# Kernel tuning notes

Hardware: AMD Instinct MI355X
Metric: run time of the kernel (lower is better)

The kernel has to match this reference:

```python
import jax, jax.numpy as jnp
import numpy as np

N_NODES = 50000
N_EDGES = 800000
N_GRAPHS = 128
IN_DIM = 128
HID = 128
OUT = 64
N_CONV = 4
BN_EPS = 1e-5


def setup_inputs() -> dict:
    key = jax.random.key(0)
    ks = jax.random.split(key, 12)
    h = jax.random.normal(ks[0], (N_NODES, IN_DIM), jnp.float32)
    edge_src = jax.random.randint(ks[1], (N_EDGES,), 0, N_NODES)
    edge_dst = jax.random.randint(ks[2], (N_EDGES,), 0, N_NODES)
    graph_ids = jnp.sort(jax.random.randint(ks[3], (N_NODES,), 0, N_GRAPHS))
    s1 = 1.0 / np.sqrt(IN_DIM)
    W1 = jax.random.uniform(ks[4], (N_CONV, IN_DIM, HID), jnp.float32, -s1, s1)
    W2 = jax.random.uniform(ks[5], (N_CONV, HID, HID), jnp.float32, -s1, s1)
    bn1_g = jnp.ones((N_CONV, HID), jnp.float32)
    bn1_b = jnp.zeros((N_CONV, HID), jnp.float32)
    bn2_g = jnp.ones((N_CONV, HID), jnp.float32)
    bn2_b = jnp.zeros((N_CONV, HID), jnp.float32)
    predW = jax.random.uniform(ks[6], (5, HID, OUT), jnp.float32, -s1, s1)
    predb = jnp.zeros((5, OUT), jnp.float32)
    return dict(h=h, edge_src=edge_src, edge_dst=edge_dst, graph_ids=graph_ids,
                W1=W1, bn1_g=bn1_g, bn1_b=bn1_b, W2=W2, bn2_g=bn2_g, bn2_b=bn2_b,
                predW=predW, predb=predb)


def _batchnorm(x, g, b):
    # training-mode batchnorm over the node dimension (biased variance, as torch)
    m = jnp.mean(x, axis=0)
    v = jnp.mean(jnp.square(x - m), axis=0)
    return (x - m) * jax.lax.rsqrt(v + BN_EPS) * g + b


def reference(h, edge_src, edge_dst, graph_ids, W1, bn1_g, bn1_b, W2, bn2_g, bn2_b, predW, predb):
    hidden_rep = [h]
    for i in range(N_CONV):
        # GINConv, eps=0: aggregate neighbor sum, add self, apply MLP
        agg = jax.ops.segment_sum(h[edge_src], edge_dst, num_segments=N_NODES)
        z = agg + h  # [N, d]
        z = jnp.matmul(z, W1[i])
        z = jax.nn.relu(_batchnorm(z, bn1_g[i], bn1_b[i]))
        z = jnp.matmul(z, W2[i])
        # outer batchnorm + relu
        h = jax.nn.relu(_batchnorm(z, bn2_g[i], bn2_b[i]))
        hidden_rep.append(h)
    score = jnp.zeros((N_GRAPHS, OUT), jnp.float32)
    for i, hi in enumerate(hidden_rep):
        pooled = jax.ops.segment_sum(hi, graph_ids, num_segments=N_GRAPHS)  # [G, d]
        score = score + jnp.matmul(pooled, predW[i]) + predb[i]
    return score
```

## Files before the change

kernel.cpp:

```cpp
#include <hip/hip_runtime.h>

#define NN 50000
#define NE 800000
#define NG 128
#define DIM 128
#define OUTD 64
#define NCONV 4
#define NB 196
#define BN_EPS 1e-5f

typedef __attribute__((ext_vector_type(8))) short short8;
typedef __attribute__((ext_vector_type(4))) float f32x4;
union BF8 { uint4 u; short8 s; };

__device__ inline unsigned f2bf(float f) {
    unsigned u = __float_as_uint(f);
    return (u + 0x7FFFu + ((u >> 16) & 1u)) >> 16;
}
__device__ inline float bf_lo(unsigned u) { return __uint_as_float(u << 16); }
__device__ inline float bf_hi(unsigned u) { return __uint_as_float(u & 0xFFFF0000u); }

__global__ __launch_bounds__(256) void k_degree(const int* __restrict__ dst,
                                                int* __restrict__ deg)
{
    int e = blockIdx.x * 256 + threadIdx.x;
    if (e < NE) atomicAdd(&deg[dst[e]], 1);
}

__global__ __launch_bounds__(256) void k_scan1(const int* __restrict__ deg,
                                               int* __restrict__ bsum)
{
    __shared__ int part[256];
    int t = threadIdx.x, idx = blockIdx.x * 256 + t;
    int v = (idx < NN) ? deg[idx] : 0;
    part[t] = v;
    __syncthreads();
    #pragma unroll
    for (int off = 1; off < 256; off <<= 1) {
        int u = (t >= off) ? part[t - off] : 0;
        __syncthreads();
        part[t] += u;
        __syncthreads();
    }
    if (t == 255) bsum[blockIdx.x] = part[255];
}

__global__ __launch_bounds__(256) void k_scan2(const int* __restrict__ bsum,
                                               int* __restrict__ boff)
{
    __shared__ int part[256];
    int t = threadIdx.x;
    int v = (t < NB) ? bsum[t] : 0;
    part[t] = v;
    __syncthreads();
    #pragma unroll
    for (int off = 1; off < 256; off <<= 1) {
        int u = (t >= off) ? part[t - off] : 0;
        __syncthreads();
        part[t] += u;
        __syncthreads();
    }
    if (t < NB) boff[t] = part[t] - v;
}

__global__ __launch_bounds__(256) void k_scan3(const int* __restrict__ deg,
                                               const int* __restrict__ boff,
                                               int* __restrict__ rowptr,
                                               int* __restrict__ cursor)
{
    __shared__ int part[256];
    int t = threadIdx.x, idx = blockIdx.x * 256 + t;
    int v = (idx < NN) ? deg[idx] : 0;
    part[t] = v;
    __syncthreads();
    #pragma unroll
    for (int off = 1; off < 256; off <<= 1) {
        int u = (t >= off) ? part[t - off] : 0;
        __syncthreads();
        part[t] += u;
        __syncthreads();
    }
    if (idx < NN) {
        int excl = part[t] - v + boff[blockIdx.x];
        rowptr[idx] = excl;
        cursor[idx] = excl;
    }
    if (idx == 0) rowptr[NN] = NE;
}

__global__ __launch_bounds__(256) void k_fill(const int* __restrict__ src,
                                              const int* __restrict__ dst,
                                              int* __restrict__ cursor,
                                              int* __restrict__ csr)
{
    int e = blockIdx.x * 256 + threadIdx.x;
    if (e >= NE) return;
    int pos = atomicAdd(&cursor[dst[e]], 1);
    csr[pos] = src[e];
}

__global__ __launch_bounds__(256) void k_bounds(const int* __restrict__ gid,
                                                int* __restrict__ gstart)
{
    int n = blockIdx.x * 256 + threadIdx.x;
    if (n >= NN) return;
    int g = gid[n];
    int gp = (n == 0) ? -1 : gid[n - 1];
    for (int x = gp + 1; x <= g; ++x) gstart[x] = n;
    if (n == NN - 1)
        for (int x = g + 1; x <= NG; ++x) gstart[x] = NN;
}

__global__ __launch_bounds__(256) void k_wprep(const float* __restrict__ W1,
                                               const float* __restrict__ W2,
                                               unsigned short* __restrict__ Wbf)
{
    int tid = blockIdx.x * 256 + threadIdx.x;
    int l   = tid & 63;
    int ctg = (tid >> 6) & 7;
    int kk  = (tid >> 9) & 3;
    int mat = tid >> 11;
    const float* Ws = (mat < 4) ? (W1 + (size_t)mat * DIM * DIM)
                                : (W2 + (size_t)(mat - 4) * DIM * DIM);
    int col = ctg * 16 + (l & 15);
    int k0  = kk * 32 + (l >> 4) * 8;
    unsigned sh[8];
    #pragma unroll
    for (int j = 0; j < 8; ++j) sh[j] = f2bf(Ws[(size_t)(k0 + j) * DIM + col]);
    uint4 pk;
    pk.x = sh[0] | (sh[1] << 16); pk.y = sh[2] | (sh[3] << 16);
    pk.z = sh[4] | (sh[5] << 16); pk.w = sh[6] | (sh[7] << 16);
    ((uint4*)Wbf)[tid] = pk;
}

__global__ __launch_bounds__(256) void k_cvt(const float* __restrict__ in,
                                             unsigned short* __restrict__ outb)
{
    int idx = blockIdx.x * 256 + threadIdx.x;
    if (idx >= NN * DIM / 4) return;
    float4 v = ((const float4*)in)[idx];
    uint2 pk;
    pk.x = f2bf(v.x) | (f2bf(v.y) << 16);
    pk.y = f2bf(v.z) | (f2bf(v.w) << 16);
    ((uint2*)outb)[idx] = pk;
}

__device__ inline void bn_affine4(const float* __restrict__ sumP,
                                  const float* __restrict__ sqP,
                                  const float* __restrict__ gP,
                                  const float* __restrict__ bP,
                                  int ch0, float4& av, float4& cv)
{
    const float invM = 1.f / (float)NN;
    #pragma unroll
    for (int j = 0; j < 4; ++j) {
        int ch = ch0 + j;
        float m = sumP[ch] * invM;
        float var = sqP[ch] * invM - m * m;
        float s = gP[ch] * rsqrtf(var + BN_EPS);
        (&av.x)[j] = s;
        (&cv.x)[j] = bP[ch] - m * s;
    }
}

__device__ inline float4 aff_relu(float4 v, const float4 av, const float4 cv)
{
    v.x = fmaxf(fmaf(v.x, av.x, cv.x), 0.f);
    v.y = fmaxf(fmaf(v.y, av.y, cv.y), 0.f);
    v.z = fmaxf(fmaf(v.z, av.z, cv.z), 0.f);
    v.w = fmaxf(fmaf(v.w, av.w, cv.w), 0.f);
    return v;
}

__global__ __launch_bounds__(256) void k_gather_bf(
    const unsigned short* __restrict__ hbf,
    const int* __restrict__ rowptr, const int* __restrict__ csr,
    unsigned short* __restrict__ aggbf)
{
    int t = threadIdx.x;
    int n = blockIdx.x * 8 + (t >> 5);
    if (n >= NN) return;
    int l = t & 31;
    const uint2* hp = (const uint2*)hbf;
    uint2 v0 = hp[(size_t)n * 32 + l];
    float a0 = bf_lo(v0.x), a1 = bf_hi(v0.x), a2 = bf_lo(v0.y), a3 = bf_hi(v0.y);
    int p = rowptr[n], end = rowptr[n + 1];
    for (; p + 4 <= end; p += 4) {
        int s0 = csr[p], s1 = csr[p + 1], s2 = csr[p + 2], s3 = csr[p + 3];
        uint2 u0 = hp[(size_t)s0 * 32 + l];
        uint2 u1 = hp[(size_t)s1 * 32 + l];
        uint2 u2 = hp[(size_t)s2 * 32 + l];
        uint2 u3 = hp[(size_t)s3 * 32 + l];
        a0 += bf_lo(u0.x) + bf_lo(u1.x) + bf_lo(u2.x) + bf_lo(u3.x);
        a1 += bf_hi(u0.x) + bf_hi(u1.x) + bf_hi(u2.x) + bf_hi(u3.x);
        a2 += bf_lo(u0.y) + bf_lo(u1.y) + bf_lo(u2.y) + bf_lo(u3.y);
        a3 += bf_hi(u0.y) + bf_hi(u1.y) + bf_hi(u2.y) + bf_hi(u3.y);
    }
    for (; p < end; ++p) {
        uint2 u = hp[(size_t)csr[p] * 32 + l];
        a0 += bf_lo(u.x); a1 += bf_hi(u.x); a2 += bf_lo(u.y); a3 += bf_hi(u.y);
    }
    uint2 pk;
    pk.x = f2bf(a0) | (f2bf(a1) << 16);
    pk.y = f2bf(a2) | (f2bf(a3) << 16);
    ((uint2*)aggbf)[(size_t)n * 32 + l] = pk;
}

template<bool AFFINE, bool WRITEH>
__global__ __launch_bounds__(256) void k_poolseg(
    const float* __restrict__ z,
    const float* __restrict__ sumP, const float* __restrict__ sqP,
    const float* __restrict__ gP, const float* __restrict__ bP,
    const int* __restrict__ gstart, float* __restrict__ pooled,
    unsigned short* __restrict__ hbf)
{
    const int g = blockIdx.x >> 2, split = blockIdx.x & 3;
    const int s = gstart[g], e = gstart[g + 1];
    const int len = e - s;
    const int chunk = (len + 3) >> 2;
    const int rs = s + split * chunk;
    const int re = min(e, rs + chunk);
    const int c4 = threadIdx.x & 31, rl = threadIdx.x >> 5;
    float4 av, cv;
    if (AFFINE) bn_affine4(sumP, sqP, gP, bP, c4 * 4, av, cv);
    float4 acc = make_float4(0.f, 0.f, 0.f, 0.f);
    for (int r = rs + rl; r < re; r += 8) {
        float4 v = ((const float4*)z)[(size_t)r * 32 + c4];
        if (AFFINE) v = aff_relu(v, av, cv);
        if (WRITEH) {
            uint2 pk;
            pk.x = f2bf(v.x) | (f2bf(v.y) << 16);
            pk.y = f2bf(v.z) | (f2bf(v.w) << 16);
            ((uint2*)(hbf + (size_t)r * DIM))[c4] = pk;
        }
        acc.x += v.x; acc.y += v.y; acc.z += v.z; acc.w += v.w;
    }
    __shared__ float4 red[8][32];
    red[rl][c4] = acc;
    __syncthreads();
    if (rl == 0) {
        float4 s4 = red[0][c4];
        #pragma unroll
        for (int r8 = 1; r8 < 8; ++r8) {
            float4 u = red[r8][c4];
            s4.x += u.x; s4.y += u.y; s4.z += u.z; s4.w += u.w;
        }
        float* p = pooled + (size_t)g * DIM + c4 * 4;
        atomicAdd(p + 0, s4.x);
        atomicAdd(p + 1, s4.y);
        atomicAdd(p + 2, s4.z);
        atomicAdd(p + 3, s4.w);
    }
}

template<bool ABF16>
__global__ __launch_bounds__(256) void k_gemm_mfma(
    const void* __restrict__ Xv_,
    const float* __restrict__ sumP, const float* __restrict__ sqP,
    const float* __restrict__ gP, const float* __restrict__ bP,
    const unsigned short* __restrict__ Wbf,
    float* __restrict__ Z,
    float* __restrict__ colsum, float* __restrict__ colsq)
{
    __shared__ unsigned short a_lds[16 * 520];
    const int t = threadIdx.x;
    const int row0 = blockIdx.x * 64;
    const int q = t & 15;

    if (ABF16) {
        const unsigned short* Xb = (const unsigned short*)Xv_;
        #pragma unroll
        for (int it = 0; it < 4; ++it) {
            int id = t + it * 256;
            int row = id >> 4;
            int grow = row0 + row;
            uint4 pk = make_uint4(0, 0, 0, 0);
            if (grow < NN) pk = ((const uint4*)(Xb + (size_t)grow * DIM))[q];
            int g = (row >> 4) * 4 + (q >> 2);
            int l = (row & 15) + (q & 3) * 16;
            *(uint4*)(a_lds + g * 520 + l * 8) = pk;
        }
    } else {
        const float* X = (const float*)Xv_;
        float av[8], cv[8];
        {
            const float invM = 1.f / (float)NN;
            #pragma unroll
            for (int j = 0; j < 8; ++j) {
                int ch = q * 8 + j;
                float m = sumP[ch] * invM;
                float var = sqP[ch] * invM - m * m;
                float sc = gP[ch] * rsqrtf(var + BN_EPS);
                av[j] = sc; cv[j] = bP[ch] - m * sc;
            }
        }
        #pragma unroll
        for (int it = 0; it < 4; ++it) {
            int id = t + it * 256;
            int row = id >> 4;
            int grow = row0 + row;
            float4 x0 = make_float4(0.f, 0.f, 0.f, 0.f), x1 = x0;
            if (grow < NN) {
                const float4* Xp = (const float4*)(X + (size_t)grow * DIM + q * 8);
                x0 = Xp[0]; x1 = Xp[1];
            }
            float xv[8] = {x0.x, x0.y, x0.z, x0.w, x1.x, x1.y, x1.z, x1.w};
            unsigned sh[8];
            #pragma unroll
            for (int j = 0; j < 8; ++j)
                sh[j] = f2bf(fmaxf(fmaf(xv[j], av[j], cv[j]), 0.f));
            uint4 pk;
            pk.x = sh[0] | (sh[1] << 16); pk.y = sh[2] | (sh[3] << 16);
            pk.z = sh[4] | (sh[5] << 16); pk.w = sh[6] | (sh[7] << 16);
            int g = (row >> 4) * 4 + (q >> 2);
            int l = (row & 15) + (q & 3) * 16;
            *(uint4*)(a_lds + g * 520 + l * 8) = pk;
        }
    }
    __syncthreads();

    const int w = t >> 6, lane = t & 63;
    const int rh = w >> 1, ch = w & 1;
    f32x4 acc[2][4];
    #pragma unroll
    for (int i = 0; i < 2; ++i)
        #pragma unroll
        for (int j = 0; j < 4; ++j) acc[i][j] = 0;

    const uint4* Wb = (const uint4*)Wbf;
    #pragma unroll
    for (int kk = 0; kk < 4; ++kk) {
        BF8 a[2], b[4];
        #pragma unroll
        for (int rti = 0; rti < 2; ++rti) {
            int g = (rh * 2 + rti) * 4 + kk;
            a[rti].u = *(const uint4*)(a_lds + g * 520 + lane * 8);
        }
        #pragma unroll
        for (int ct = 0; ct < 4; ++ct)
            b[ct].u = Wb[(kk * 8 + ch * 4 + ct) * 64 + lane];
        #pragma unroll
        for (int rti = 0; rti < 2; ++rti)
            #pragma unroll
            for (int ct = 0; ct < 4; ++ct)
                acc[rti][ct] = __builtin_amdgcn_mfma_f32_16x16x32_bf16(
                    a[rti].s, b[ct].s, acc[rti][ct], 0, 0, 0);
    }

    float ps[4] = {0.f, 0.f, 0.f, 0.f}, pq[4] = {0.f, 0.f, 0.f, 0.f};
    #pragma unroll
    for (int rti = 0; rti < 2; ++rti) {
        #pragma unroll
        for (int r = 0; r < 4; ++r) {
            int grow = row0 + rh * 32 + rti * 16 + (lane >> 4) * 4 + r;
            if (grow < NN) {
                #pragma unroll
                for (int ct = 0; ct < 4; ++ct) {
                    float v = acc[rti][ct][r];
                    Z[(size_t)grow * DIM + ch * 64 + ct * 16 + (lane & 15)] = v;
                    ps[ct] += v;
                    pq[ct] += v * v;
                }
            }
        }
    }
    __syncthreads();
    float* red = (float*)a_lds;
    red[t] = 0.f;
    __syncthreads();
    #pragma unroll
    for (int ct = 0; ct < 4; ++ct) {
        int col = ch * 64 + ct * 16 + (lane & 15);
        atomicAdd(&red[col], ps[ct]);
        atomicAdd(&red[128 + col], pq[ct]);
    }
    __syncthreads();
    if (t < DIM) {
        atomicAdd(colsum + t, red[t]);
        atomicAdd(colsq + t, red[128 + t]);
    }
}

__global__ __launch_bounds__(320) void k_score(const float* __restrict__ pooled,
                                               const float* __restrict__ predW,
                                               const float* __restrict__ predb,
                                               float* __restrict__ out)
{
    __shared__ float red[5][OUTD];
    const int g = blockIdx.x;
    const int w = threadIdx.x >> 6;
    const int o = threadIdx.x & 63;
    const float* pr = pooled + (size_t)w * NG * DIM + (size_t)g * DIM;
    const float* Wp = predW + (size_t)w * DIM * OUTD;
    float acc = predb[w * OUTD + o];
    #pragma unroll 8
    for (int k = 0; k < DIM; ++k) acc = fmaf(pr[k], Wp[k * OUTD + o], acc);
    red[w][o] = acc;
    __syncthreads();
    if (threadIdx.x < OUTD) {
        float s = red[0][o] + red[1][o] + red[2][o] + red[3][o] + red[4][o];
        out[(size_t)g * OUTD + o] = s;
    }
}

extern "C" void kernel_launch(void* const* d_in, const int* in_sizes, int n_in,
                              void* d_out, int out_size, void* d_ws, size_t ws_size,
                              hipStream_t stream)
{
    const float* h     = (const float*)d_in[0];
    const int*   esrc  = (const int*)d_in[1];
    const int*   edst  = (const int*)d_in[2];
    const int*   gid   = (const int*)d_in[3];
    const float* W1    = (const float*)d_in[4];
    const float* bn1g  = (const float*)d_in[5];
    const float* bn1b  = (const float*)d_in[6];
    const float* W2    = (const float*)d_in[7];
    const float* bn2g  = (const float*)d_in[8];
    const float* bn2b  = (const float*)d_in[9];
    const float* predW = (const float*)d_in[10];
    const float* predb = (const float*)d_in[11];
    float* out = (float*)d_out;

    float* ws = (float*)d_ws;
    const size_t NF = (size_t)NN * DIM;
    float* z1     = ws;
    float* Zb     = ws + NF;
    float* pooled = ws + 2 * NF;
    float* stats  = pooled + 5 * NG * DIM;

    unsigned short* hbf   = (unsigned short*)(stats + NCONV * 1024);
    unsigned short* aggbf = hbf + NF;
    unsigned short* Wbf   = aggbf + NF;
    int* ideg   = (int*)(Wbf + 8 * 16384);
    int* rowptr = ideg + NN;
    int* cursor = rowptr + NN + 1;
    int* csr    = cursor + NN;
    int* gstart = csr + NE;
    int* bsum   = gstart + NG + 1;
    int* boff   = bsum + NB;

    hipMemsetAsync(pooled, 0, (5 * NG * DIM + NCONV * 1024) * sizeof(float), stream);
    hipMemsetAsync(ideg, 0, NN * sizeof(int), stream);

    k_wprep<<<64, 256, 0, stream>>>(W1, W2, Wbf);
    k_cvt<<<(NN * DIM / 4 + 255) / 256, 256, 0, stream>>>(h, hbf);
    k_degree<<<(NE + 255) / 256, 256, 0, stream>>>(edst, ideg);
    k_scan1<<<NB, 256, 0, stream>>>(ideg, bsum);
    k_scan2<<<1, 256, 0, stream>>>(bsum, boff);
    k_scan3<<<NB, 256, 0, stream>>>(ideg, boff, rowptr, cursor);
    k_fill<<<(NE + 255) / 256, 256, 0, stream>>>(esrc, edst, cursor, csr);
    k_bounds<<<(NN + 255) / 256, 256, 0, stream>>>(gid, gstart);

    k_poolseg<false, false><<<NG * 4, 256, 0, stream>>>(
        h, nullptr, nullptr, nullptr, nullptr, gstart, pooled, nullptr);

    const int GB = (NN + 63) / 64;
    for (int i = 0; i < NCONV; ++i) {
        float* st = stats + i * 1024;
        k_gather_bf<<<(NN + 7) / 8, 256, 0, stream>>>(hbf, rowptr, csr, aggbf);
        k_gemm_mfma<true><<<GB, 256, 0, stream>>>(
            aggbf, nullptr, nullptr, nullptr, nullptr,
            Wbf + (size_t)i * 16384, z1, st, st + 128);
        k_gemm_mfma<false><<<GB, 256, 0, stream>>>(
            z1, st, st + 128, bn1g + i * DIM, bn1b + i * DIM,
            Wbf + (size_t)(4 + i) * 16384, Zb, st + 512, st + 640);
        if (i < NCONV - 1)
            k_poolseg<true, true><<<NG * 4, 256, 0, stream>>>(
                Zb, st + 512, st + 640, bn2g + i * DIM, bn2b + i * DIM,
                gstart, pooled + (size_t)(i + 1) * NG * DIM, hbf);
        else
            k_poolseg<true, false><<<NG * 4, 256, 0, stream>>>(
                Zb, st + 512, st + 640, bn2g + i * DIM, bn2b + i * DIM,
                gstart, pooled + (size_t)(i + 1) * NG * DIM, nullptr);
    }

    k_score<<<NG, 320, 0, stream>>>(pooled, predW, predb, out);
}
```

Measured before the change: 624.0 us.

## Fuse neighbor gather into first GEMM and store intermediates as bf16

The separate gather kernel is removed. The first MFMA GEMM now performs the CSR neighbor sum while staging its A tile into LDS, so the aggbf buffer is no longer written and read back. The GEMM outputs z1 and z2 are stored as bf16 instead of fp32, which halves their write and read traffic in the next GEMM and in the pooling kernel. In exchange, the gather now runs with 16 threads per row, each loading 16-byte chunks, inside a GEMM block of 64 rows. This may give less memory-level parallelism than the old 8-rows-per-block gather, and adds bf16 rounding of the pre-batchnorm activations.

```diff
diff --git a/kernel.cpp b/kernel.cpp
--- a/kernel.cpp
+++ b/kernel.cpp
@@ -172,43 +172,9 @@
     return v;
 }
 
-__global__ __launch_bounds__(256) void k_gather_bf(
-    const unsigned short* __restrict__ hbf,
-    const int* __restrict__ rowptr, const int* __restrict__ csr,
-    unsigned short* __restrict__ aggbf)
-{
-    int t = threadIdx.x;
-    int n = blockIdx.x * 8 + (t >> 5);
-    if (n >= NN) return;
-    int l = t & 31;
-    const uint2* hp = (const uint2*)hbf;
-    uint2 v0 = hp[(size_t)n * 32 + l];
-    float a0 = bf_lo(v0.x), a1 = bf_hi(v0.x), a2 = bf_lo(v0.y), a3 = bf_hi(v0.y);
-    int p = rowptr[n], end = rowptr[n + 1];
-    for (; p + 4 <= end; p += 4) {
-        int s0 = csr[p], s1 = csr[p + 1], s2 = csr[p + 2], s3 = csr[p + 3];
-        uint2 u0 = hp[(size_t)s0 * 32 + l];
-        uint2 u1 = hp[(size_t)s1 * 32 + l];
-        uint2 u2 = hp[(size_t)s2 * 32 + l];
-        uint2 u3 = hp[(size_t)s3 * 32 + l];
-        a0 += bf_lo(u0.x) + bf_lo(u1.x) + bf_lo(u2.x) + bf_lo(u3.x);
-        a1 += bf_hi(u0.x) + bf_hi(u1.x) + bf_hi(u2.x) + bf_hi(u3.x);
-        a2 += bf_lo(u0.y) + bf_lo(u1.y) + bf_lo(u2.y) + bf_lo(u3.y);
-        a3 += bf_hi(u0.y) + bf_hi(u1.y) + bf_hi(u2.y) + bf_hi(u3.y);
-    }
-    for (; p < end; ++p) {
-        uint2 u = hp[(size_t)csr[p] * 32 + l];
-        a0 += bf_lo(u.x); a1 += bf_hi(u.x); a2 += bf_lo(u.y); a3 += bf_hi(u.y);
-    }
-    uint2 pk;
-    pk.x = f2bf(a0) | (f2bf(a1) << 16);
-    pk.y = f2bf(a2) | (f2bf(a3) << 16);
-    ((uint2*)aggbf)[(size_t)n * 32 + l] = pk;
-}
-
-template<bool AFFINE, bool WRITEH>
+template<bool AFFINE, bool WRITEH, bool INBF16>
 __global__ __launch_bounds__(256) void k_poolseg(
-    const float* __restrict__ z,
+    const void* __restrict__ z_,
     const float* __restrict__ sumP, const float* __restrict__ sqP,
     const float* __restrict__ gP, const float* __restrict__ bP,
     const int* __restrict__ gstart, float* __restrict__ pooled,
@@ -225,7 +191,13 @@
     if (AFFINE) bn_affine4(sumP, sqP, gP, bP, c4 * 4, av, cv);
     float4 acc = make_float4(0.f, 0.f, 0.f, 0.f);
     for (int r = rs + rl; r < re; r += 8) {
-        float4 v = ((const float4*)z)[(size_t)r * 32 + c4];
+        float4 v;
+        if (INBF16) {
+            uint2 w = ((const uint2*)z_)[(size_t)r * 32 + c4];
+            v = make_float4(bf_lo(w.x), bf_hi(w.x), bf_lo(w.y), bf_hi(w.y));
+        } else {
+            v = ((const float4*)z_)[(size_t)r * 32 + c4];
+        }
         if (AFFINE) v = aff_relu(v, av, cv);
         if (WRITEH) {
             uint2 pk;
@@ -253,13 +225,14 @@
     }
 }
 
-template<bool ABF16>
+template<bool GATHER, bool AFFINE>
 __global__ __launch_bounds__(256) void k_gemm_mfma(
-    const void* __restrict__ Xv_,
+    const unsigned short* __restrict__ Xb,
+    const int* __restrict__ rowptr, const int* __restrict__ csr,
     const float* __restrict__ sumP, const float* __restrict__ sqP,
     const float* __restrict__ gP, const float* __restrict__ bP,
     const unsigned short* __restrict__ Wbf,
-    float* __restrict__ Z,
+    unsigned short* __restrict__ Z,
     float* __restrict__ colsum, float* __restrict__ colsq)
 {
     __shared__ unsigned short a_lds[16 * 520];
@@ -267,55 +240,68 @@
     const int row0 = blockIdx.x * 64;
     const int q = t & 15;
 
-    if (ABF16) {
-        const unsigned short* Xb = (const unsigned short*)Xv_;
-        #pragma unroll
-        for (int it = 0; it < 4; ++it) {
-            int id = t + it * 256;
-            int row = id >> 4;
-            int grow = row0 + row;
-            uint4 pk = make_uint4(0, 0, 0, 0);
-            if (grow < NN) pk = ((const uint4*)(Xb + (size_t)grow * DIM))[q];
-            int g = (row >> 4) * 4 + (q >> 2);
-            int l = (row & 15) + (q & 3) * 16;
-            *(uint4*)(a_lds + g * 520 + l * 8) = pk;
-        }
-    } else {
-        const float* X = (const float*)Xv_;
-        float av[8], cv[8];
-        {
-            const float invM = 1.f / (float)NN;
-            #pragma unroll
-            for (int j = 0; j < 8; ++j) {
-                int ch = q * 8 + j;
-                float m = sumP[ch] * invM;
-                float var = sqP[ch] * invM - m * m;
-                float sc = gP[ch] * rsqrtf(var + BN_EPS);
-                av[j] = sc; cv[j] = bP[ch] - m * sc;
+    float av[8], cv[8];
+    if (AFFINE) {
+        const float invM = 1.f / (float)NN;
+        #pragma unroll
+        for (int j = 0; j < 8; ++j) {
+            int ch = q * 8 + j;
+            float m = sumP[ch] * invM;
+            float var = sqP[ch] * invM - m * m;
+            float sc = gP[ch] * rsqrtf(var + BN_EPS);
+            av[j] = sc; cv[j] = bP[ch] - m * sc;
+        }
+    }
+
+    const uint4* hp4 = (const uint4*)Xb;
+    #pragma unroll
+    for (int it = 0; it < 4; ++it) {
+        int row = (t >> 4) + it * 16;
+        int grow = row0 + row;
+        uint4 pk = make_uint4(0, 0, 0, 0);
+        if (grow < NN) {
+            float a[8];
+            uint4 v = hp4[(size_t)grow * 16 + q];
+            a[0] = bf_lo(v.x); a[1] = bf_hi(v.x);
+            a[2] = bf_lo(v.y); a[3] = bf_hi(v.y);
+            a[4] = bf_lo(v.z); a[5] = bf_hi(v.z);
+            a[6] = bf_lo(v.w); a[7] = bf_hi(v.w);
+            if (GATHER) {
+                int p = rowptr[grow], end = rowptr[grow + 1];
+                for (; p + 2 <= end; p += 2) {
+                    int s0 = csr[p], s1 = csr[p + 1];
+                    uint4 u0 = hp4[(size_t)s0 * 16 + q];
+                    uint4 u1 = hp4[(size_t)s1 * 16 + q];
+                    a[0] += bf_lo(u0.x) + bf_lo(u1.x);
+                    a[1] += bf_hi(u0.x) + bf_hi(u1.x);
+                    a[2] += bf_lo(u0.y) + bf_lo(u1.y);
+                    a[3] += bf_hi(u0.y) + bf_hi(u1.y);
+                    a[4] += bf_lo(u0.z) + bf_lo(u1.z);
+                    a[5] += bf_hi(u0.z) + bf_hi(u1.z);
+                    a[6] += bf_lo(u0.w) + bf_lo(u1.w);
+                    a[7] += bf_hi(u0.w) + bf_hi(u1.w);
+                }
+                if (p < end) {
+                    uint4 u = hp4[(size_t)csr[p] * 16 + q];
+                    a[0] += bf_lo(u.x); a[1] += bf_hi(u.x);
+                    a[2] += bf_lo(u.y); a[3] += bf_hi(u.y);
+                    a[4] += bf_lo(u.z); a[5] += bf_hi(u.z);
+                    a[6] += bf_lo(u.w); a[7] += bf_hi(u.w);
+                }
             }
-        }
-        #pragma unroll
-        for (int it = 0; it < 4; ++it) {
-            int id = t + it * 256;
-            int row = id >> 4;
-            int grow = row0 + row;
-            float4 x0 = make_float4(0.f, 0.f, 0.f, 0.f), x1 = x0;
-            if (grow < NN) {
-                const float4* Xp = (const float4*)(X + (size_t)grow * DIM + q * 8);
-                x0 = Xp[0]; x1 = Xp[1];
+            if (AFFINE) {
+                #pragma unroll
+                for (int j = 0; j < 8; ++j)
+                    a[j] = fmaxf(fmaf(a[j], av[j], cv[j]), 0.f);
             }
-            float xv[8] = {x0.x, x0.y, x0.z, x0.w, x1.x, x1.y, x1.z, x1.w};
-            unsigned sh[8];
-            #pragma unroll
-            for (int j = 0; j < 8; ++j)
-                sh[j] = f2bf(fmaxf(fmaf(xv[j], av[j], cv[j]), 0.f));
-            uint4 pk;
-            pk.x = sh[0] | (sh[1] << 16); pk.y = sh[2] | (sh[3] << 16);
-            pk.z = sh[4] | (sh[5] << 16); pk.w = sh[6] | (sh[7] << 16);
-            int g = (row >> 4) * 4 + (q >> 2);
-            int l = (row & 15) + (q & 3) * 16;
-            *(uint4*)(a_lds + g * 520 + l * 8) = pk;
-        }
+            pk.x = f2bf(a[0]) | (f2bf(a[1]) << 16);
+            pk.y = f2bf(a[2]) | (f2bf(a[3]) << 16);
+            pk.z = f2bf(a[4]) | (f2bf(a[5]) << 16);
+            pk.w = f2bf(a[6]) | (f2bf(a[7]) << 16);
+        }
+        int g = (row >> 4) * 4 + (q >> 2);
+        int l = (row & 15) + (q & 3) * 16;
+        *(uint4*)(a_lds + g * 520 + l * 8) = pk;
     }
     __syncthreads();
 
@@ -357,7 +343,8 @@
                 #pragma unroll
                 for (int ct = 0; ct < 4; ++ct) {
                     float v = acc[rti][ct][r];
-                    Z[(size_t)grow * DIM + ch * 64 + ct * 16 + (lane & 15)] = v;
+                    Z[(size_t)grow * DIM + ch * 64 + ct * 16 + (lane & 15)] =
+                        (unsigned short)f2bf(v);
                     ps[ct] += v;
                     pq[ct] += v * v;
                 }
@@ -423,14 +410,13 @@
 
     float* ws = (float*)d_ws;
     const size_t NF = (size_t)NN * DIM;
-    float* z1     = ws;
-    float* Zb     = ws + NF;
-    float* pooled = ws + 2 * NF;
+    float* pooled = ws;
     float* stats  = pooled + 5 * NG * DIM;
 
-    unsigned short* hbf   = (unsigned short*)(stats + NCONV * 1024);
-    unsigned short* aggbf = hbf + NF;
-    unsigned short* Wbf   = aggbf + NF;
+    unsigned short* hbf  = (unsigned short*)(stats + NCONV * 1024);
+    unsigned short* z1b  = hbf + NF;
+    unsigned short* z2b  = z1b + NF;
+    unsigned short* Wbf  = z2b + NF;
     int* ideg   = (int*)(Wbf + 8 * 16384);
     int* rowptr = ideg + NN;
     int* cursor = rowptr + NN + 1;
@@ -451,26 +437,25 @@
     k_fill<<<(NE + 255) / 256, 256, 0, stream>>>(esrc, edst, cursor, csr);
     k_bounds<<<(NN + 255) / 256, 256, 0, stream>>>(gid, gstart);
 
-    k_poolseg<false, false><<<NG * 4, 256, 0, stream>>>(
+    k_poolseg<false, false, false><<<NG * 4, 256, 0, stream>>>(
         h, nullptr, nullptr, nullptr, nullptr, gstart, pooled, nullptr);
 
     const int GB = (NN + 63) / 64;
     for (int i = 0; i < NCONV; ++i) {
         float* st = stats + i * 1024;
-        k_gather_bf<<<(NN + 7) / 8, 256, 0, stream>>>(hbf, rowptr, csr, aggbf);
-        k_gemm_mfma<true><<<GB, 256, 0, stream>>>(
-            aggbf, nullptr, nullptr, nullptr, nullptr,
-            Wbf + (size_t)i * 16384, z1, st, st + 128);
-        k_gemm_mfma<false><<<GB, 256, 0, stream>>>(
-            z1, st, st + 128, bn1g + i * DIM, bn1b + i * DIM,
-            Wbf + (size_t)(4 + i) * 16384, Zb, st + 512, st + 640);
+        k_gemm_mfma<true, false><<<GB, 256, 0, stream>>>(
+            hbf, rowptr, csr, nullptr, nullptr, nullptr, nullptr,
+            Wbf + (size_t)i * 16384, z1b, st, st + 128);
+        k_gemm_mfma<false, true><<<GB, 256, 0, stream>>>(
+            z1b, nullptr, nullptr, st, st + 128, bn1g + i * DIM, bn1b + i * DIM,
+            Wbf + (size_t)(4 + i) * 16384, z2b, st + 512, st + 640);
         if (i < NCONV - 1)
-            k_poolseg<true, true><<<NG * 4, 256, 0, stream>>>(
-                Zb, st + 512, st + 640, bn2g + i * DIM, bn2b + i * DIM,
+            k_poolseg<true, true, true><<<NG * 4, 256, 0, stream>>>(
+                z2b, st + 512, st + 640, bn2g + i * DIM, bn2b + i * DIM,
                 gstart, pooled + (size_t)(i + 1) * NG * DIM, hbf);
         else
-            k_poolseg<true, false><<<NG * 4, 256, 0, stream>>>(
-                Zb, st + 512, st + 640, bn2g + i * DIM, bn2b + i * DIM,
+            k_poolseg<true, false, true><<<NG * 4, 256, 0, stream>>>(
+                z2b, st + 512, st + 640, bn2g + i * DIM, bn2b + i * DIM,
                 gstart, pooled + (size_t)(i + 1) * NG * DIM, nullptr);
     }
 
```

Result: no change. 618.4 us (-0.9%).
